# Optimization experiments

Hardware: AMD Instinct MI355X
Metric: run time of the kernel (lower is better)

## Reference

```python
import jax, jax.numpy as jnp
import numpy as np

N = 50000      # nodes
E = 800000     # edges (avg degree 16)
D = 128        # in_dim == hidden_dim
CD = 3         # coord_dim (SE(3))
L = 3          # num_layers


def setup_inputs() -> dict:
    key = jax.random.key(0)
    ks = jax.random.split(key, 10)
    s = np.float32(1.0 / np.sqrt(D))
    return {
        "x": jax.random.normal(ks[0], (N, D), jnp.float32),
        "pos": jax.random.normal(ks[1], (N, CD), jnp.float32),
        "edge_index": jax.random.randint(ks[2], (2, E), 0, N, dtype=jnp.int32),
        # per-layer stacked params (in_dim == hidden_dim so all layers stack)
        "Wl": jax.random.normal(ks[3], (L, D, D), jnp.float32) * s,
        "bl": jnp.zeros((L, D), jnp.float32),
        "Wc": jax.random.normal(ks[4], (L, D, 1), jnp.float32) * s,
        "bc": jnp.zeros((L, 1), jnp.float32),
        "WR": jax.random.normal(ks[5], (L, D, CD * CD), jnp.float32) * s,
        "bR": jnp.zeros((L, CD * CD), jnp.float32),
        "Wt": jax.random.normal(ks[6], (L, D, CD), jnp.float32) * s,
        "bt": jnp.zeros((L, CD), jnp.float32),
        # final fc
        "Wf": jax.random.normal(ks[7], (D, D), jnp.float32) * s,
        "bf": jnp.zeros((D,), jnp.float32),
    }


def reference(x, pos, edge_index, Wl, bl, Wc, bc, WR, bR, Wt, bt, Wf, bf):
    src, dst = edge_index[0], edge_index[1]
    n = x.shape[0]
    # R defaults to identity, t to zeros (R_dict/t_dict None path)
    R = jnp.broadcast_to(jnp.eye(CD, dtype=x.dtype), (n, CD, CD))
    t = jnp.zeros_like(pos)
    for i in range(L):
        h = x @ Wl[i] + bl[i]                          # (N, D)  per-edge-type linear
        # MessagePassing aggr='add': message x_j = h[src], scatter-add at dst
        out = jax.ops.segment_sum(h[src], dst, num_segments=n)  # (N, D)
        pos = pos + (out @ Wc[i] + bc[i])              # (N,3) + (N,1) broadcast
        R_upd = (out @ WR[i] + bR[i]).reshape(n, CD, CD)
        Q = jnp.linalg.qr(R_upd)[0]                    # orthonormalize rotation update
        R = Q @ R
        t = t + (out @ Wt[i] + bt[i])
        x = out
    z = x @ Wf + bf
    return z, pos, R, t
```

## Files before the change

kernel.cpp:

```cpp
#include <hip/hip_runtime.h>
#include <hip/hip_fp16.h>

typedef _Float16 half8 __attribute__((ext_vector_type(8)));
typedef float floatx4 __attribute__((ext_vector_type(4)));

#define OSH 13

__device__ inline void qr3_q(const double A[3][3], double Q[3][3]){
  double a[3][3];
#pragma unroll
  for (int r = 0; r < 3; r++)
#pragma unroll
    for (int c = 0; c < 3; c++) a[r][c] = A[r][c];

  double v1[3] = {1.0, 0.0, 0.0};
  double tau1 = 0.0;
  {
    double xn2 = a[1][0]*a[1][0] + a[2][0]*a[2][0];
    if (xn2 != 0.0){
      double alpha = a[0][0];
      double beta = -copysign(sqrt(alpha*alpha + xn2), alpha);
      tau1 = (beta - alpha) / beta;
      double inv = 1.0 / (alpha - beta);
      v1[1] = a[1][0] * inv;
      v1[2] = a[2][0] * inv;
#pragma unroll
      for (int c = 1; c < 3; c++){
        double w = a[0][c] + v1[1]*a[1][c] + v1[2]*a[2][c];
        double tw = tau1 * w;
        a[0][c] -= tw;
        a[1][c] -= tw * v1[1];
        a[2][c] -= tw * v1[2];
      }
    }
  }
  double tau2 = 0.0, v2 = 0.0;
  {
    double x2 = a[2][1];
    if (x2 != 0.0){
      double alpha = a[1][1];
      double beta = -copysign(sqrt(alpha*alpha + x2*x2), alpha);
      tau2 = (beta - alpha) / beta;
      v2 = x2 / (alpha - beta);
    }
  }
  double M[3][3] = {{1.0, 0.0, 0.0},
                    {0.0, 1.0 - tau2, -tau2*v2},
                    {0.0, -tau2*v2, 1.0 - tau2*v2*v2}};
#pragma unroll
  for (int c = 0; c < 3; c++){
    double w = v1[0]*M[0][c] + v1[1]*M[1][c] + v1[2]*M[2][c];
#pragma unroll
    for (int r = 0; r < 3; r++)
      Q[r][c] = M[r][c] - tau1 * v1[r] * w;
  }
}

__device__ inline void se3_node_ds(int n, const float ds[13],
                                   const float* __restrict__ bc, const float* __restrict__ bR,
                                   const float* __restrict__ bt, const float* __restrict__ pos_in,
                                   float* __restrict__ pos_o, float* __restrict__ R_o,
                                   float* __restrict__ t_o, int layer){
  double A[3][3], Q[3][3];
#pragma unroll
  for (int r = 0; r < 3; r++)
#pragma unroll
    for (int c = 0; c < 3; c++)
      A[r][c] = (double)ds[1 + r*3 + c] + (double)bR[r*3 + c];
  qr3_q(A, Q);

  double pd = (double)ds[0] + (double)bc[0];
#pragma unroll
  for (int c = 0; c < 3; c++){
    double base = (layer == 0) ? (double)pos_in[n*3 + c] : (double)pos_o[n*3 + c];
    pos_o[n*3 + c] = (float)(base + pd);
  }

  if (layer == 0){
#pragma unroll
    for (int r = 0; r < 3; r++)
#pragma unroll
      for (int c = 0; c < 3; c++)
        R_o[n*9 + r*3 + c] = (float)Q[r][c];
  } else {
    double Rold[3][3];
#pragma unroll
    for (int r = 0; r < 3; r++)
#pragma unroll
      for (int c = 0; c < 3; c++)
        Rold[r][c] = (double)R_o[n*9 + r*3 + c];
#pragma unroll
    for (int r = 0; r < 3; r++)
#pragma unroll
      for (int c = 0; c < 3; c++){
        double s = Q[r][0]*Rold[0][c] + Q[r][1]*Rold[1][c] + Q[r][2]*Rold[2][c];
        R_o[n*9 + r*3 + c] = (float)s;
      }
  }
#pragma unroll
  for (int c = 0; c < 3; c++){
    double base = (layer == 0) ? 0.0 : (double)t_o[n*3 + c];
    t_o[n*3 + c] = (float)(base + (double)ds[10 + c] + (double)bt[c]);
  }
}

__launch_bounds__(256)
__global__ void k_pre(const float* __restrict__ x, _Float16* __restrict__ o, int N,
                      const float* __restrict__ Wl, const float* __restrict__ Wf,
                      const float* __restrict__ Wc, const float* __restrict__ WR,
                      const float* __restrict__ Wt, _Float16* __restrict__ wTx,
                      _Float16* __restrict__ wHd,
                      int* __restrict__ cursor, int nbuck, int cvtB){
  const int b = blockIdx.x;
  if (b < cvtB){
    int c = b*256 + threadIdx.x;
    if (c >= (N+1)*16) return;
    int n = c >> 4;
    half8 h = {};
    if (n < N){
      const float* p = x + (size_t)c*8;
      float4 f0 = *(const float4*)p;
      float4 f1 = *(const float4*)(p + 4);
      h[0]=(_Float16)f0.x; h[1]=(_Float16)f0.y; h[2]=(_Float16)f0.z; h[3]=(_Float16)f0.w;
      h[4]=(_Float16)f1.x; h[5]=(_Float16)f1.y; h[6]=(_Float16)f1.z; h[7]=(_Float16)f1.w;
    }
    *(half8*)(o + (size_t)c*8) = h;
    return;
  }
  if (b == cvtB && threadIdx.x < nbuck) cursor[threadIdx.x] = 0;
  int t = (b - cvtB)*256 + threadIdx.x;
  if (t < 4*128*128){
    int l = t >> 14;
    int n = (t >> 7) & 127;
    int k = t & 127;
    const float* W = (l < 3) ? (Wl + (size_t)l*16384) : Wf;
    wTx[t] = (_Float16)W[k*128 + n];
  } else if (t < 4*128*128 + 3*16*128){
    int u = t - 4*128*128;
    int l = u >> 11;
    int r = u & 2047;
    int n = r >> 7;
    int k = r & 127;
    float v = 0.f;
    if (n == 0)      v = Wc[(size_t)l*128 + k];
    else if (n < 10) v = WR[(size_t)l*1152 + k*9 + (n-1)];
    else if (n < 13) v = Wt[(size_t)l*384 + k*3 + (n-10)];
    wHd[u] = (_Float16)v;
  }
}

__launch_bounds__(256)
__global__ void k_bin(const int* __restrict__ src, const int* __restrict__ dst,
                      int E, int nbuck, int capB,
                      int* __restrict__ cursor, int* __restrict__ binned){
  __shared__ int cnt[128];
  __shared__ int segbase[128];
  const int tid = threadIdx.x;
  for (int t = tid; t < nbuck; t += 256) cnt[t] = 0;
  __syncthreads();
  const int e0 = blockIdx.x*4096 + tid;
  int pk[16], bk[16];
#pragma unroll
  for (int j = 0; j < 16; j++){
    int e = e0 + j*256;
    if (e < E){
      int d = dst[e], s = src[e];
      bk[j] = d >> 9;
      pk[j] = (s << 9) | (d & 511);
      atomicAdd(&cnt[bk[j]], 1);
    } else bk[j] = -1;
  }
  __syncthreads();
  for (int t = tid; t < nbuck; t += 256){
    int c = cnt[t];
    if (c > 0) segbase[t] = t*capB + atomicAdd(&cursor[t], c);
    cnt[t] = 0;
  }
  __syncthreads();
#pragma unroll
  for (int j = 0; j < 16; j++){
    if (bk[j] >= 0){
      int ord = atomicAdd(&cnt[bk[j]], 1);
      binned[segbase[bk[j]] + ord] = pk[j];
    }
  }
}

__launch_bounds__(256)
__global__ void k_build(const int* __restrict__ binned, const int* __restrict__ cursor,
                        int N, int capB, int capC,
                        int2* __restrict__ sd, int* __restrict__ csr){
  __shared__ int deg2[512*8];
  __shared__ int lst2[512*8];
  __shared__ int cnt2[512*8];
  __shared__ int scn[256];
  const int b = blockIdx.x, tid = threadIdx.x;
  for (int t = tid; t < 512*8; t += 256){ deg2[t] = 0; cnt2[t] = 0; }
  __syncthreads();
  const int nE = cursor[b];
  const int gbase = b*capB;
  for (int i = tid; i < nE; i += 256){
    int v = binned[gbase + i];
    int o = v >> (9 + OSH);
    if (o > 7) o = 7;
    atomicAdd(&deg2[((v & 511) << 3) + o], 1);
  }
  __syncthreads();
  int d0 = 0, d1 = 0;
#pragma unroll
  for (int o = 0; o < 8; o++){ d0 += deg2[((2*tid) << 3) + o]; d1 += deg2[((2*tid+1) << 3) + o]; }
  const int p0 = (d0+7)&~7, p1 = (d1+7)&~7;
  scn[tid] = p0 + p1;
  __syncthreads();
#pragma unroll
  for (int off = 1; off < 256; off <<= 1){
    int add = (tid >= off) ? scn[tid-off] : 0;
    __syncthreads();
    scn[tid] += add;
    __syncthreads();
  }
  const int ex = scn[tid] - (p0 + p1);
  const int csrb = b*capC;
  {
    int off0 = ex;
#pragma unroll
    for (int o = 0; o < 8; o++){ lst2[((2*tid) << 3) + o] = off0; off0 += deg2[((2*tid) << 3) + o]; }
    int off1 = ex + p0;
#pragma unroll
    for (int o = 0; o < 8; o++){ lst2[((2*tid+1) << 3) + o] = off1; off1 += deg2[((2*tid+1) << 3) + o]; }
  }
  const int n0 = b*512 + 2*tid, n1 = n0 + 1;
  if (n0 < N) sd[n0] = make_int2(csrb + ex, (d0 << 16) | p0);
  if (n1 < N) sd[n1] = make_int2(csrb + ex + p0, (d1 << 16) | p1);
  __syncthreads();
  for (int i = tid; i < nE; i += 256){
    int v = binned[gbase + i];
    int dl = v & 511, s = v >> 9;
    int o = s >> OSH; if (o > 7) o = 7;
    int ord = atomicAdd(&cnt2[(dl << 3) + o], 1);
    csr[csrb + lst2[(dl << 3) + o] + ord] = s;
  }
  for (int j = d0; j < p0; j++) csr[csrb + ex + j] = N;
  for (int j = d1; j < p1; j++) csr[csrb + ex + p0 + j] = N;
}

__launch_bounds__(256)
__global__ void k_fused(const _Float16* __restrict__ Xin,
                        const _Float16* __restrict__ Wmain,
                        const _Float16* __restrict__ Whd,
                        const float* __restrict__ bias,
                        const int* __restrict__ csr, const int2* __restrict__ sd,
                        _Float16* __restrict__ Out,
                        int N, int layer,
                        const float* __restrict__ bc, const float* __restrict__ bR,
                        const float* __restrict__ bt, const float* __restrict__ pos_in,
                        float* __restrict__ pos_o, float* __restrict__ R_o,
                        float* __restrict__ t_o){
  __shared__ __align__(16) _Float16 lg[64][136];
  __shared__ __align__(16) float lheads[64*16];
  __shared__ float ldeg[64];

  const int tid  = threadIdx.x;
  const int wave = tid >> 6;
  const int lane = tid & 63;
  const int quad = lane >> 4;
  const int l16  = lane & 15;
  const int rbase0 = blockIdx.x*64;

  {
    const int nbase = rbase0 + wave*16;
    int nn = nbase + (lane & 15);
    int2 sv = (nn < N) ? sd[nn] : make_int2(0, 0);
    const unsigned int* Xu = (const unsigned int*)Xin;
    for (int i = 0; i < 16; i++){
      int s0    = __builtin_amdgcn_readlane(sv.x, i);
      int dpack = __builtin_amdgcn_readlane(sv.y, i);
      int degp  = dpack & 0xffff;
      if (lane == 0) ldeg[wave*16 + i] = (float)(dpack >> 16);
      float acc0 = 0.f, acc1 = 0.f;
      for (int base = 0; base < degp; base += 64){
        int myidx = csr[s0 + base + lane];
        int m = degp - base; m = (m < 64) ? m : 64;
        for (int k = 0; k < m; k += 8){
          unsigned int v[8];
#pragma unroll
          for (int j = 0; j < 8; j++){
            int idx = __builtin_amdgcn_readlane(myidx, k + j);
            v[j] = Xu[(size_t)idx*64 + lane];
          }
#pragma unroll
          for (int j = 0; j < 8; j++){
            float2 f = __half22float2(*(__half2*)&v[j]);
            acc0 += f.x; acc1 += f.y;
          }
        }
      }
      __half2 ho = __floats2half2_rn(acc0, acc1);
      ((unsigned int*)&lg[wave*16 + i][0])[lane] = *(unsigned int*)&ho;
    }
  }
  __syncthreads();

  const int cthi = wave >> 1;
  half8 af[4][2];
#pragma unroll
  for (int kc = 0; kc < 4; kc++)
#pragma unroll
    for (int rt = 0; rt < 2; rt++){
      int rl = (wave & 1)*32 + rt*16 + l16;
      af[kc][rt] = *(const half8*)&lg[rl][kc*32 + quad*8];
    }
  __syncthreads();

  floatx4 acc[2][4] = {};
#pragma unroll
  for (int kc = 0; kc < 4; kc++)
#pragma unroll
    for (int ct = 0; ct < 4; ct++){
      half8 bf = *(const half8*)(Wmain + (size_t)((cthi*4 + ct)*16 + l16)*128 + kc*32 + quad*8);
      acc[0][ct] = __builtin_amdgcn_mfma_f32_16x16x32_f16(af[kc][0], bf, acc[0][ct], 0, 0, 0);
      acc[1][ct] = __builtin_amdgcn_mfma_f32_16x16x32_f16(af[kc][1], bf, acc[1][ct], 0, 0, 0);
    }

#pragma unroll
  for (int rt = 0; rt < 2; rt++){
    float dgv[4];
#pragma unroll
    for (int reg = 0; reg < 4; reg++)
      dgv[reg] = ldeg[(wave & 1)*32 + rt*16 + quad*4 + reg];
#pragma unroll
    for (int ct = 0; ct < 4; ct++){
      int col = (cthi*4 + ct)*16 + l16;
      float b = bias[col];
#pragma unroll
      for (int reg = 0; reg < 4; reg++){
        int rl = (wave & 1)*32 + rt*16 + quad*4 + reg;
        lg[rl][col] = (_Float16)(acc[rt][ct][reg] + b*dgv[reg]);
      }
    }
  }
  __syncthreads();

#pragma unroll
  for (int i = 0; i < 4; i++){
    int idx8 = i*256 + tid;
    int row = idx8 >> 4, c8 = idx8 & 15;
    int gr = rbase0 + row;
    if (gr < N){
      *(half8*)(Out + (size_t)gr*128 + c8*8) = *(const half8*)&lg[row][c8*8];
    } else if (gr == N){
      half8 z = {};
      *(half8*)(Out + (size_t)gr*128 + c8*8) = z;
    }
  }

  {
    floatx4 hacc = {};
#pragma unroll
    for (int kc = 0; kc < 4; kc++){
      half8 ha = *(const half8*)&lg[wave*16 + l16][kc*32 + quad*8];
      half8 bf = *(const half8*)(Whd + (size_t)l16*128 + kc*32 + quad*8);
      hacc = __builtin_amdgcn_mfma_f32_16x16x32_f16(ha, bf, hacc, 0, 0, 0);
    }
#pragma unroll
    for (int reg = 0; reg < 4; reg++)
      lheads[(wave*16 + quad*4 + reg)*16 + l16] = hacc[reg];
  }
  __syncthreads();

  if (tid < 64){
    int n = rbase0 + tid;
    if (n < N){
      float ds[13];
#pragma unroll
      for (int c = 0; c < 13; c++) ds[c] = lheads[tid*16 + c];
      se3_node_ds(n, ds, bc, bR, bt, pos_in, pos_o, R_o, t_o, layer);
    }
  }
}

__launch_bounds__(256)
__global__ void k_fused_fin(const _Float16* __restrict__ Xin,
                        const _Float16* __restrict__ Wmain,
                        const _Float16* __restrict__ Whd,
                        const float* __restrict__ bias,
                        const int* __restrict__ csr, const int2* __restrict__ sd,
                        int N, int layer,
                        const float* __restrict__ bc, const float* __restrict__ bR,
                        const float* __restrict__ bt, const float* __restrict__ pos_in,
                        float* __restrict__ pos_o, float* __restrict__ R_o,
                        float* __restrict__ t_o,
                        const _Float16* __restrict__ Wfin,
                        const float* __restrict__ bfin,
                        float* __restrict__ Zout){
  __shared__ __align__(16) _Float16 lg[64][136];
  __shared__ __align__(16) float lheads[64*16];
  __shared__ float ldeg[64];

  const int tid  = threadIdx.x;
  const int wave = tid >> 6;
  const int lane = tid & 63;
  const int quad = lane >> 4;
  const int l16  = lane & 15;
  const int rbase0 = blockIdx.x*64;

  {
    const int nbase = rbase0 + wave*16;
    int nn = nbase + (lane & 15);
    int2 sv = (nn < N) ? sd[nn] : make_int2(0, 0);
    const unsigned int* Xu = (const unsigned int*)Xin;
    for (int i = 0; i < 16; i++){
      int s0    = __builtin_amdgcn_readlane(sv.x, i);
      int dpack = __builtin_amdgcn_readlane(sv.y, i);
      int degp  = dpack & 0xffff;
      if (lane == 0) ldeg[wave*16 + i] = (float)(dpack >> 16);
      float acc0 = 0.f, acc1 = 0.f;
      for (int base = 0; base < degp; base += 64){
        int myidx = csr[s0 + base + lane];
        int m = degp - base; m = (m < 64) ? m : 64;
        for (int k = 0; k < m; k += 8){
          unsigned int v[8];
#pragma unroll
          for (int j = 0; j < 8; j++){
            int idx = __builtin_amdgcn_readlane(myidx, k + j);
            v[j] = Xu[(size_t)idx*64 + lane];
          }
#pragma unroll
          for (int j = 0; j < 8; j++){
            float2 f = __half22float2(*(__half2*)&v[j]);
            acc0 += f.x; acc1 += f.y;
          }
        }
      }
      __half2 ho = __floats2half2_rn(acc0, acc1);
      ((unsigned int*)&lg[wave*16 + i][0])[lane] = *(unsigned int*)&ho;
    }
  }
  __syncthreads();

  const int cthi = wave >> 1;
  half8 af[4][2];
#pragma unroll
  for (int kc = 0; kc < 4; kc++)
#pragma unroll
    for (int rt = 0; rt < 2; rt++){
      int rl = (wave & 1)*32 + rt*16 + l16;
      af[kc][rt] = *(const half8*)&lg[rl][kc*32 + quad*8];
    }
  __syncthreads();

  floatx4 acc[2][4] = {};
#pragma unroll
  for (int kc = 0; kc < 4; kc++)
#pragma unroll
    for (int ct = 0; ct < 4; ct++){
      half8 bf = *(const half8*)(Wmain + (size_t)((cthi*4 + ct)*16 + l16)*128 + kc*32 + quad*8);
      acc[0][ct] = __builtin_amdgcn_mfma_f32_16x16x32_f16(af[kc][0], bf, acc[0][ct], 0, 0, 0);
      acc[1][ct] = __builtin_amdgcn_mfma_f32_16x16x32_f16(af[kc][1], bf, acc[1][ct], 0, 0, 0);
    }

#pragma unroll
  for (int rt = 0; rt < 2; rt++){
    float dgv[4];
#pragma unroll
    for (int reg = 0; reg < 4; reg++)
      dgv[reg] = ldeg[(wave & 1)*32 + rt*16 + quad*4 + reg];
#pragma unroll
    for (int ct = 0; ct < 4; ct++){
      int col = (cthi*4 + ct)*16 + l16;
      float b = bias[col];
#pragma unroll
      for (int reg = 0; reg < 4; reg++){
        int rl = (wave & 1)*32 + rt*16 + quad*4 + reg;
        lg[rl][col] = (_Float16)(acc[rt][ct][reg] + b*dgv[reg]);
      }
    }
  }
  __syncthreads();

  {
    half8 zf[4][2];
#pragma unroll
    for (int kc = 0; kc < 4; kc++)
#pragma unroll
      for (int rt = 0; rt < 2; rt++){
        int rl = (wave & 1)*32 + rt*16 + l16;
        zf[kc][rt] = *(const half8*)&lg[rl][kc*32 + quad*8];
      }
    floatx4 zacc[2][4] = {};
#pragma unroll
    for (int kc = 0; kc < 4; kc++)
#pragma unroll
      for (int ct = 0; ct < 4; ct++){
        half8 bf = *(const half8*)(Wfin + (size_t)((cthi*4 + ct)*16 + l16)*128 + kc*32 + quad*8);
        zacc[0][ct] = __builtin_amdgcn_mfma_f32_16x16x32_f16(zf[kc][0], bf, zacc[0][ct], 0, 0, 0);
        zacc[1][ct] = __builtin_amdgcn_mfma_f32_16x16x32_f16(zf[kc][1], bf, zacc[1][ct], 0, 0, 0);
      }
#pragma unroll
    for (int rt = 0; rt < 2; rt++)
#pragma unroll
      for (int ct = 0; ct < 4; ct++){
        int col = (cthi*4 + ct)*16 + l16;
        float b = bfin[col];
#pragma unroll
        for (int reg = 0; reg < 4; reg++){
          int gr = rbase0 + (wave & 1)*32 + rt*16 + quad*4 + reg;
          if (gr < N) Zout[(size_t)gr*128 + col] = zacc[rt][ct][reg] + b;
        }
      }
  }

  {
    floatx4 hacc = {};
#pragma unroll
    for (int kc = 0; kc < 4; kc++){
      half8 ha = *(const half8*)&lg[wave*16 + l16][kc*32 + quad*8];
      half8 bf = *(const half8*)(Whd + (size_t)l16*128 + kc*32 + quad*8);
      hacc = __builtin_amdgcn_mfma_f32_16x16x32_f16(ha, bf, hacc, 0, 0, 0);
    }
#pragma unroll
    for (int reg = 0; reg < 4; reg++)
      lheads[(wave*16 + quad*4 + reg)*16 + l16] = hacc[reg];
  }
  __syncthreads();

  if (tid < 64){
    int n = rbase0 + tid;
    if (n < N){
      float ds[13];
#pragma unroll
      for (int c = 0; c < 13; c++) ds[c] = lheads[tid*16 + c];
      se3_node_ds(n, ds, bc, bR, bt, pos_in, pos_o, R_o, t_o, layer);
    }
  }
}

extern "C" void kernel_launch(void* const* d_in, const int* in_sizes, int n_in,
                              void* d_out, int out_size, void* d_ws, size_t ws_size,
                              hipStream_t stream){
  const float* x0  = (const float*)d_in[0];
  const float* pos = (const float*)d_in[1];
  const int*   ei  = (const int*)d_in[2];
  const float* Wl  = (const float*)d_in[3];
  const float* bl  = (const float*)d_in[4];
  const float* Wc  = (const float*)d_in[5];
  const float* bc  = (const float*)d_in[6];
  const float* WR  = (const float*)d_in[7];
  const float* bR  = (const float*)d_in[8];
  const float* Wt  = (const float*)d_in[9];
  const float* bt  = (const float*)d_in[10];
  const float* Wf  = (const float*)d_in[11];
  const float* bf  = (const float*)d_in[12];

  const int N = in_sizes[0] / 128;
  const int E = in_sizes[2] / 2;
  const int* srcp = ei;
  const int* dstp = ei + E;

  float* z_out = (float*)d_out;
  float* pos_o = z_out + (size_t)N*128;
  float* R_o   = pos_o + (size_t)N*3;
  float* t_o   = R_o   + (size_t)N*9;

  const int nbuck = (N + 511) >> 9;
  const int capB  = (((E + nbuck - 1)/nbuck)*5/4 + 256 + 63) & ~63;
  const int capC  = capB + 512*7;

  char* ws = (char*)d_ws;
  size_t off = 0;
  auto alloc = [&](size_t bytes)->char*{
    char* p = ws + off; off += (bytes + 511) & ~(size_t)511; return p;
  };
  _Float16* bufA = (_Float16*)alloc((size_t)(N+1)*128*2);
  _Float16* bufB = (_Float16*)alloc((size_t)(N+1)*128*2);
  _Float16* wTx  = (_Float16*)alloc((size_t)4*128*128*2);
  _Float16* wHd  = (_Float16*)alloc((size_t)3*16*128*2);
  int2*  sd     = (int2*) alloc((size_t)N*8);
  int*   cursor = (int*)  alloc((size_t)nbuck*4);
  int*   binned = (int*)  alloc((size_t)nbuck*capB*4);
  int*   csr    = (int*)  alloc((size_t)nbuck*capC*4);

  const int cvtB = ((N+1)*16 + 255)/256;
  const int prep_total = 4*128*128 + 3*16*128;
  const int prepB = (prep_total + 255)/256;
  k_pre<<<dim3(cvtB + prepB), dim3(256), 0, stream>>>(
      x0, bufA, N, Wl, Wf, Wc, WR, Wt, wTx, wHd, cursor, nbuck, cvtB);
  k_bin   <<<dim3((E + 4095)/4096), dim3(256), 0, stream>>>(srcp, dstp, E, nbuck, capB, cursor, binned);
  k_build <<<dim3(nbuck), dim3(256), 0, stream>>>(binned, cursor, N, capB, capC, sd, csr);

  const int fused_blocks = (N + 64) >> 6;

  k_fused<<<dim3(fused_blocks), dim3(256), 0, stream>>>(
      bufA, wTx, wHd, bl,
      csr, sd, bufB, N, 0,
      bc, bR, bt, pos, pos_o, R_o, t_o);
  k_fused<<<dim3(fused_blocks), dim3(256), 0, stream>>>(
      bufB, wTx + (size_t)16384, wHd + (size_t)2048, bl + 128,
      csr, sd, bufA, N, 1,
      bc + 1, bR + 9, bt + 3, pos, pos_o, R_o, t_o);
  k_fused_fin<<<dim3(fused_blocks), dim3(256), 0, stream>>>(
      bufA, wTx + (size_t)2*16384, wHd + (size_t)2*2048, bl + 256,
      csr, sd, N, 2,
      bc + 2, bR + 18, bt + 6, pos, pos_o, R_o, t_o,
      wTx + (size_t)3*16384, bf, z_out);
}
```

Measured before the change: 277.2 us.

## Merge conversion and edge binning into one launch, shrink CSR buckets to 128 nodes

```diff
diff --git a/kernel.cpp b/kernel.cpp
--- a/kernel.cpp
+++ b/kernel.cpp
@@ -5,6 +5,8 @@
 typedef float floatx4 __attribute__((ext_vector_type(4)));
 
 #define OSH 13
+#define BN  128
+#define BSH 7
 
 __device__ inline void qr3_q(const double A[3][3], double Q[3][3]){
   double a[3][3];
@@ -105,15 +107,22 @@
 }
 
 __launch_bounds__(256)
-__global__ void k_pre(const float* __restrict__ x, _Float16* __restrict__ o, int N,
-                      const float* __restrict__ Wl, const float* __restrict__ Wf,
-                      const float* __restrict__ Wc, const float* __restrict__ WR,
-                      const float* __restrict__ Wt, _Float16* __restrict__ wTx,
-                      _Float16* __restrict__ wHd,
-                      int* __restrict__ cursor, int nbuck, int cvtB){
+__global__ void k_prebin(const float* __restrict__ x, _Float16* __restrict__ o, int N,
+                         const float* __restrict__ Wl, const float* __restrict__ Wf,
+                         const float* __restrict__ Wc, const float* __restrict__ WR,
+                         const float* __restrict__ Wt, _Float16* __restrict__ wTx,
+                         _Float16* __restrict__ wHd,
+                         const int* __restrict__ src, const int* __restrict__ dst,
+                         int E, int nbuck, int capB,
+                         int* __restrict__ cursor, int* __restrict__ binned,
+                         int cvtB, int prepB){
+  __shared__ int cnt[512];
+  __shared__ int segbase[512];
   const int b = blockIdx.x;
+  const int tid = threadIdx.x;
+
   if (b < cvtB){
-    int c = b*256 + threadIdx.x;
+    int c = b*256 + tid;
     if (c >= (N+1)*16) return;
     int n = c >> 4;
     half8 h = {};
@@ -127,46 +136,41 @@
     *(half8*)(o + (size_t)c*8) = h;
     return;
   }
-  if (b == cvtB && threadIdx.x < nbuck) cursor[threadIdx.x] = 0;
-  int t = (b - cvtB)*256 + threadIdx.x;
-  if (t < 4*128*128){
-    int l = t >> 14;
-    int n = (t >> 7) & 127;
-    int k = t & 127;
-    const float* W = (l < 3) ? (Wl + (size_t)l*16384) : Wf;
-    wTx[t] = (_Float16)W[k*128 + n];
-  } else if (t < 4*128*128 + 3*16*128){
-    int u = t - 4*128*128;
-    int l = u >> 11;
-    int r = u & 2047;
-    int n = r >> 7;
-    int k = r & 127;
-    float v = 0.f;
-    if (n == 0)      v = Wc[(size_t)l*128 + k];
-    else if (n < 10) v = WR[(size_t)l*1152 + k*9 + (n-1)];
-    else if (n < 13) v = Wt[(size_t)l*384 + k*3 + (n-10)];
-    wHd[u] = (_Float16)v;
-  }
-}
-
-__launch_bounds__(256)
-__global__ void k_bin(const int* __restrict__ src, const int* __restrict__ dst,
-                      int E, int nbuck, int capB,
-                      int* __restrict__ cursor, int* __restrict__ binned){
-  __shared__ int cnt[128];
-  __shared__ int segbase[128];
-  const int tid = threadIdx.x;
+  if (b < cvtB + prepB){
+    int t = (b - cvtB)*256 + tid;
+    if (t < 4*128*128){
+      int l = t >> 14;
+      int n = (t >> 7) & 127;
+      int k = t & 127;
+      const float* W = (l < 3) ? (Wl + (size_t)l*16384) : Wf;
+      wTx[t] = (_Float16)W[k*128 + n];
+    } else if (t < 4*128*128 + 3*16*128){
+      int u = t - 4*128*128;
+      int l = u >> 11;
+      int r = u & 2047;
+      int n = r >> 7;
+      int k = r & 127;
+      float v = 0.f;
+      if (n == 0)      v = Wc[(size_t)l*128 + k];
+      else if (n < 10) v = WR[(size_t)l*1152 + k*9 + (n-1)];
+      else if (n < 13) v = Wt[(size_t)l*384 + k*3 + (n-10)];
+      wHd[u] = (_Float16)v;
+    }
+    return;
+  }
+
+  const int bb = b - cvtB - prepB;
   for (int t = tid; t < nbuck; t += 256) cnt[t] = 0;
   __syncthreads();
-  const int e0 = blockIdx.x*4096 + tid;
+  const int e0 = bb*4096 + tid;
   int pk[16], bk[16];
 #pragma unroll
   for (int j = 0; j < 16; j++){
     int e = e0 + j*256;
     if (e < E){
       int d = dst[e], s = src[e];
-      bk[j] = d >> 9;
-      pk[j] = (s << 9) | (d & 511);
+      bk[j] = d >> BSH;
+      pk[j] = (s << BSH) | (d & (BN-1));
       atomicAdd(&cnt[bk[j]], 1);
     } else bk[j] = -1;
   }
@@ -190,58 +194,60 @@
 __global__ void k_build(const int* __restrict__ binned, const int* __restrict__ cursor,
                         int N, int capB, int capC,
                         int2* __restrict__ sd, int* __restrict__ csr){
-  __shared__ int deg2[512*8];
-  __shared__ int lst2[512*8];
-  __shared__ int cnt2[512*8];
-  __shared__ int scn[256];
+  __shared__ int deg2[BN*8];
+  __shared__ int lst2[BN*8];
+  __shared__ int cnt2[BN*8];
+  __shared__ int scn[BN];
   const int b = blockIdx.x, tid = threadIdx.x;
-  for (int t = tid; t < 512*8; t += 256){ deg2[t] = 0; cnt2[t] = 0; }
+  for (int t = tid; t < BN*8; t += 256){ deg2[t] = 0; cnt2[t] = 0; }
   __syncthreads();
   const int nE = cursor[b];
   const int gbase = b*capB;
   for (int i = tid; i < nE; i += 256){
     int v = binned[gbase + i];
-    int o = v >> (9 + OSH);
-    if (o > 7) o = 7;
-    atomicAdd(&deg2[((v & 511) << 3) + o], 1);
-  }
-  __syncthreads();
-  int d0 = 0, d1 = 0;
-#pragma unroll
-  for (int o = 0; o < 8; o++){ d0 += deg2[((2*tid) << 3) + o]; d1 += deg2[((2*tid+1) << 3) + o]; }
-  const int p0 = (d0+7)&~7, p1 = (d1+7)&~7;
-  scn[tid] = p0 + p1;
-  __syncthreads();
-#pragma unroll
-  for (int off = 1; off < 256; off <<= 1){
-    int add = (tid >= off) ? scn[tid-off] : 0;
+    int s = v >> BSH;
+    int o = s >> OSH; if (o > 7) o = 7;
+    atomicAdd(&deg2[((v & (BN-1)) << 3) + o], 1);
+  }
+  __syncthreads();
+  int d0 = 0, p0 = 0;
+  if (tid < BN){
+#pragma unroll
+    for (int o = 0; o < 8; o++) d0 += deg2[(tid << 3) + o];
+    p0 = (d0+7)&~7;
+    scn[tid] = p0;
+  }
+  __syncthreads();
+#pragma unroll
+  for (int off = 1; off < BN; off <<= 1){
+    int add = 0;
+    if (tid < BN && tid >= off) add = scn[tid-off];
     __syncthreads();
-    scn[tid] += add;
+    if (tid < BN) scn[tid] += add;
     __syncthreads();
   }
-  const int ex = scn[tid] - (p0 + p1);
   const int csrb = b*capC;
-  {
+  int ex = 0;
+  if (tid < BN){
+    ex = scn[tid] - p0;
     int off0 = ex;
 #pragma unroll
-    for (int o = 0; o < 8; o++){ lst2[((2*tid) << 3) + o] = off0; off0 += deg2[((2*tid) << 3) + o]; }
-    int off1 = ex + p0;
-#pragma unroll
-    for (int o = 0; o < 8; o++){ lst2[((2*tid+1) << 3) + o] = off1; off1 += deg2[((2*tid+1) << 3) + o]; }
-  }
-  const int n0 = b*512 + 2*tid, n1 = n0 + 1;
-  if (n0 < N) sd[n0] = make_int2(csrb + ex, (d0 << 16) | p0);
-  if (n1 < N) sd[n1] = make_int2(csrb + ex + p0, (d1 << 16) | p1);
+    for (int o = 0; o < 8; o++){ lst2[(tid << 3) + o] = off0; off0 += deg2[(tid << 3) + o]; }
+    int n0 = b*BN + tid;
+    if (n0 < N) sd[n0] = make_int2(csrb + ex, (d0 << 16) | p0);
+  }
   __syncthreads();
   for (int i = tid; i < nE; i += 256){
     int v = binned[gbase + i];
-    int dl = v & 511, s = v >> 9;
+    int dl = v & (BN-1), s = v >> BSH;
     int o = s >> OSH; if (o > 7) o = 7;
     int ord = atomicAdd(&cnt2[(dl << 3) + o], 1);
     csr[csrb + lst2[(dl << 3) + o] + ord] = s;
   }
-  for (int j = d0; j < p0; j++) csr[csrb + ex + j] = N;
-  for (int j = d1; j < p1; j++) csr[csrb + ex + p0 + j] = N;
+  __syncthreads();
+  if (tid < BN){
+    for (int j = d0; j < p0; j++) csr[csrb + ex + j] = N;
+  }
 }
 
 __launch_bounds__(256)
@@ -562,9 +568,9 @@
   float* R_o   = pos_o + (size_t)N*3;
   float* t_o   = R_o   + (size_t)N*9;
 
-  const int nbuck = (N + 511) >> 9;
+  const int nbuck = (N + BN - 1) >> BSH;
   const int capB  = (((E + nbuck - 1)/nbuck)*5/4 + 256 + 63) & ~63;
-  const int capC  = capB + 512*7;
+  const int capC  = capB + BN*7;
 
   char* ws = (char*)d_ws;
   size_t off = 0;
@@ -583,10 +589,13 @@
   const int cvtB = ((N+1)*16 + 255)/256;
   const int prep_total = 4*128*128 + 3*16*128;
   const int prepB = (prep_total + 255)/256;
-  k_pre<<<dim3(cvtB + prepB), dim3(256), 0, stream>>>(
-      x0, bufA, N, Wl, Wf, Wc, WR, Wt, wTx, wHd, cursor, nbuck, cvtB);
-  k_bin   <<<dim3((E + 4095)/4096), dim3(256), 0, stream>>>(srcp, dstp, E, nbuck, capB, cursor, binned);
-  k_build <<<dim3(nbuck), dim3(256), 0, stream>>>(binned, cursor, N, capB, capC, sd, csr);
+  const int binB  = (E + 4095)/4096;
+
+  hipMemsetAsync(cursor, 0, (size_t)nbuck*4, stream);
+  k_prebin<<<dim3(cvtB + prepB + binB), dim3(256), 0, stream>>>(
+      x0, bufA, N, Wl, Wf, Wc, WR, Wt, wTx, wHd,
+      srcp, dstp, E, nbuck, capB, cursor, binned, cvtB, prepB);
+  k_build<<<dim3(nbuck), dim3(256), 0, stream>>>(binned, cursor, N, capB, capC, sd, csr);
 
   const int fused_blocks = (N + 64) >> 6;
 
```

After: 267.9 us. 1.03x faster.
